# Performance work log

Hardware: AMD Instinct MI355X
Metric: run time of the kernel (lower is better)

The kernel has to match this reference:

```python
import jax, jax.numpy as jnp
import numpy as np

B, D, K, P = 4096, 510, 128, 332


def setup_inputs() -> dict:
    key = jax.random.key(0)
    k0, k1, k2, k3, k4 = jax.random.split(key, 5)
    z = jax.random.normal(k0, (B, D), dtype=jnp.float32)
    z_pre = jax.random.normal(k1, (B, D), dtype=jnp.float32)
    codebook = jax.random.normal(k2, (K, D), dtype=jnp.float32)
    phrase_table = jax.random.normal(k3, (P, D), dtype=jnp.float32)
    position_number = jax.random.randint(k4, (B,), 0, P, dtype=jnp.int64)
    return {"z": z, "z_pre": z_pre, "codebook": codebook,
            "phrase_table": phrase_table, "position_number": position_number}


def _vq(z, codebook):
    # squared L2 distance via ||z||^2 + ||c||^2 - 2 z.c  (same argmin as tf.norm)
    d2 = (jnp.sum(z * z, axis=-1, keepdims=True)
          + jnp.sum(codebook * codebook, axis=-1)[None, :]
          - 2.0 * jnp.einsum('bd,kd->bk', z, codebook))  # [B, K]
    k = jnp.argmin(d2, axis=-1)                           # [B]
    return codebook[k]                                    # gather -> [B, D]


def reference(z, z_pre, codebook, phrase_table, position_number):
    z_q = _vq(z, codebook)
    z_pre_q = _vq(z_pre, codebook)
    phrase_emb = phrase_table[position_number]            # [B, D]
    combined = z_q + z_pre_q + phrase_emb                 # decoder input in original model
    return combined
```

## Files before the change

### kernel.cpp

```cpp
#include <hip/hip_runtime.h>


#define BHALF 4096
#define D 510
#define K_CODES 128
#define CHB 32768
#define NCHUNK 8
#define GRID 512

using f32x4  = __attribute__((ext_vector_type(4))) float;
using bf16x8 = __attribute__((ext_vector_type(8))) short;

__device__ __forceinline__ unsigned short f2bf(float f) {
    union { float f; unsigned int u; } v; v.f = f;
    return (unsigned short)((v.u + 0x7FFFu + ((v.u >> 16) & 1u)) >> 16);
}
__device__ __forceinline__ float bf2f(unsigned short h) {
    union { unsigned int u; float f; } v; v.u = ((unsigned int)h) << 16;
    return v.f;
}
__device__ __forceinline__ bool lexlt(float va, int ia, float vb, int ib) {
    return va < vb || (va == vb && ia < ib);
}
#define MFMA16 __builtin_amdgcn_mfma_f32_16x16x32_bf16

__global__ void prep_kernel(const float* __restrict__ cb,
                            float* __restrict__ cnorm,
                            char* __restrict__ img) {
    const int code = blockIdx.x;
    const int l = threadIdx.x;
    const int swz = (code & 7) << 4;
    float s = 0.f;
    #pragma unroll
    for (int i = 0; i < 8; ++i) {
        const int k = l + 64 * i;
        const float v = (k < D) ? cb[(size_t)code * D + k] : 0.f;
        s = fmaf(v, v, s);
        const unsigned short hi = f2bf(v);
        const unsigned short lo = f2bf(v - bf2f(hi));
        char* base = img + (size_t)(k >> 6) * CHB + code * 256;
        const int off = (((k & 63) * 2) ^ swz);
        *(unsigned short*)(base + off) = hi;
        *(unsigned short*)(base + 128 + off) = lo;
    }
    #pragma unroll
    for (int m = 1; m < 64; m <<= 1) s += __shfl_xor(s, m, 64);
    if (l == 0) cnorm[code] = s;
}

__launch_bounds__(512, 4)
__global__ void main_kernel(const float* __restrict__ z,
                            const float* __restrict__ zp,
                            const float* __restrict__ cb,
                            const float* __restrict__ ph,
                            const int* __restrict__ pos,
                            const float* __restrict__ cnorm,
                            const char* __restrict__ img,
                            float* __restrict__ out) {
    __shared__ __align__(1024) char lds[65536];

    const int tid  = threadIdx.x;
    const int lane = tid & 63;
    const int wu   = __builtin_amdgcn_readfirstlane(tid >> 6);
    const int l15  = lane & 15;
    const int kq   = lane >> 4;
    const int r0   = blockIdx.x * 8;
    const int code = wu * 16 + l15;
    const int swz  = (l15 & 7) << 4;
    const float cn0 = cnorm[code];

    #pragma unroll
    for (int i = 0; i < 4; ++i) {
        const int u = tid + 512 * i;
        const int row = u >> 7;
        const int col = (u & 127) * 4;
        const float* src = (row < 8) ? z + (size_t)(r0 + row) * D
                                     : zp + (size_t)(r0 + row - 8) * D;
        const float2 va = *(const float2*)(src + col);
        const float2 vb = (col + 2 < D) ? *(const float2*)(src + col + 2)
                                        : make_float2(0.f, 0.f);
        const unsigned short h0 = f2bf(va.x), h1 = f2bf(va.y),
                             h2 = f2bf(vb.x), h3 = f2bf(vb.y);
        const unsigned short g0 = f2bf(va.x - bf2f(h0)), g1 = f2bf(va.y - bf2f(h1)),
                             g2 = f2bf(vb.x - bf2f(h2)), g3 = f2bf(vb.y - bf2f(h3));
        uint2 hi2, lo2;
        hi2.x = (unsigned)h0 | ((unsigned)h1 << 16);
        hi2.y = (unsigned)h2 | ((unsigned)h3 << 16);
        lo2.x = (unsigned)g0 | ((unsigned)g1 << 16);
        lo2.y = (unsigned)g2 | ((unsigned)g3 << 16);
        const int off = row * 1024 + ((col * 2) ^ ((row & 7) << 4));
        *(uint2*)(lds + off) = hi2;
        *(uint2*)(lds + 16384 + off) = lo2;
    }

    f32x4 acc = {0.f, 0.f, 0.f, 0.f};
    const char* zh0 = lds + l15 * 1024;
    const char* zl0 = lds + 16384 + l15 * 1024;
    const char* cbrow = lds + 32768 + code * 256;

    for (int c = 0; c < NCHUNK; ++c) {
        __syncthreads();
        {
            const char* g = img + (size_t)c * CHB;
            #pragma unroll
            for (int i = 0; i < 4; ++i) {
                const int u = i * 512 + tid;
                __builtin_amdgcn_global_load_lds(
                    (const __attribute__((address_space(1))) void*)(g + (size_t)u * 16),
                    (__attribute__((address_space(3))) void*)
                        (lds + 32768 + (size_t)(i * 512 + (tid & ~63)) * 16),
                    16, 0, 0);
            }
        }
        __syncthreads();
        #pragma unroll
        for (int ks = 0; ks < 2; ++ks) {
            const int kzB = (c * 128 + ks * 64 + kq * 16) ^ swz;
            const int kcB = (ks * 64 + kq * 16) ^ swz;
            const bf16x8 a_h = *(const bf16x8*)(zh0 + kzB);
            const bf16x8 a_l = *(const bf16x8*)(zl0 + kzB);
            const bf16x8 b_h = *(const bf16x8*)(cbrow + kcB);
            const bf16x8 b_l = *(const bf16x8*)(cbrow + 128 + kcB);
            acc = MFMA16(a_h, b_h, acc, 0, 0, 0);
            acc = MFMA16(a_h, b_l, acc, 0, 0, 0);
            acc = MFMA16(a_l, b_h, acc, 0, 0, 0);
        }
    }
    __syncthreads();

    float* tv1 = (float*)(lds);
    int*   ti1 = (int*)  (lds + 512);
    float* tv2 = (float*)(lds + 1024);
    int*   ti2 = (int*)  (lds + 1536);
    int*   i1a = (int*)  (lds + 2048);
    int*   i2a = (int*)  (lds + 2112);
    float* refd= (float*)(lds + 2176);
    int*   kbf = (int*)  (lds + 2304);

    #pragma unroll
    for (int j = 0; j < 4; ++j) {
        float v1 = cn0 - 2.f * acc[j];
        int   i1 = code;
        float v2 = 3.4e38f;
        int   i2 = 1 << 30;
        #pragma unroll
        for (int m = 1; m < 16; m <<= 1) {
            const float o1 = __shfl_xor(v1, m, 64); const int oi1 = __shfl_xor(i1, m, 64);
            const float o2 = __shfl_xor(v2, m, 64); const int oi2 = __shfl_xor(i2, m, 64);
            if (lexlt(o1, oi1, v1, i1)) {
                if (lexlt(v1, i1, o2, oi2)) { v2 = v1; i2 = i1; }
                else                        { v2 = o2; i2 = oi2; }
                v1 = o1; i1 = oi1;
            } else if (lexlt(o1, oi1, v2, i2)) { v2 = o1; i2 = oi1; }
        }
        if (l15 == 0) {
            const int mrow = kq * 4 + j;
            tv1[wu * 16 + mrow] = v1; ti1[wu * 16 + mrow] = i1;
            tv2[wu * 16 + mrow] = v2; ti2[wu * 16 + mrow] = i2;
        }
    }
    __syncthreads();

    if (tid < 16) {
        float v1 = tv1[tid]; int i1 = ti1[tid];
        float v2 = tv2[tid]; int i2 = ti2[tid];
        #pragma unroll
        for (int w = 1; w < 8; ++w) {
            const float o1 = tv1[w * 16 + tid], o2 = tv2[w * 16 + tid];
            const int  oi1 = ti1[w * 16 + tid], oi2 = ti2[w * 16 + tid];
            if (lexlt(o1, oi1, v1, i1)) {
                if (lexlt(v1, i1, o2, oi2)) { v2 = v1; i2 = i1; }
                else                        { v2 = o2; i2 = oi2; }
                v1 = o1; i1 = oi1;
            } else if (lexlt(o1, oi1, v2, i2)) { v2 = o1; i2 = oi1; }
        }
        i1a[tid] = i1; i2a[tid] = i2;
    }
    __syncthreads();

    {
        const int job = tid >> 4;
        const int l16 = tid & 15;
        const int row = job >> 1;
        const int cand = (job & 1) ? i2a[row] : i1a[row];
        const float* zr = (row < 8) ? z + (size_t)(r0 + row) * D
                                    : zp + (size_t)(r0 + row - 8) * D;
        const float* cr = cb + (size_t)cand * D;
        float dot = 0.f;
        #pragma unroll
        for (int t = 0; t < 16; ++t) {
            const int col = l16 * 2 + t * 32;
            if (col < D) {
                const float2 a = *(const float2*)(zr + col);
                const float2 b = *(const float2*)(cr + col);
                dot = fmaf(a.x, b.x, fmaf(a.y, b.y, dot));
            }
        }
        #pragma unroll
        for (int m = 1; m < 16; m <<= 1) dot += __shfl_xor(dot, m, 64);
        if (l16 == 0) refd[job] = cnorm[cand] - 2.f * dot;
    }
    __syncthreads();
    if (tid < 16) {
        const float da = refd[tid * 2], db = refd[tid * 2 + 1];
        const int ia = i1a[tid], ib = i2a[tid];
        kbf[tid] = lexlt(db, ib, da, ia) ? ib : ia;
    }
    __syncthreads();

    {
        const int grow = wu;
        const int kz   = kbf[grow];
        const int kzp2 = kbf[8 + grow];
        const int pp   = pos[r0 + grow];
        const float* ra = cb + (size_t)kz * D;
        const float* rb = cb + (size_t)kzp2 * D;
        const float* rp = ph + (size_t)pp * D;
        float* ro = out + (size_t)(r0 + grow) * D;
        #pragma unroll
        for (int q = 0; q < 4; ++q) {
            const int col = lane * 8 + q * 2;
            if (col < D) {
                const float2 a = *(const float2*)(ra + col);
                const float2 b = *(const float2*)(rb + col);
                const float2 p = *(const float2*)(rp + col);
                float2 o; o.x = a.x + b.x + p.x; o.y = a.y + b.y + p.y;
                *(float2*)(ro + col) = o;
            }
        }
    }
}

extern "C" void kernel_launch(void* const* d_in, const int* in_sizes, int n_in,
                              void* d_out, int out_size, void* d_ws, size_t ws_size,
                              hipStream_t stream) {
    const float* z  = (const float*)d_in[0];
    const float* zp = (const float*)d_in[1];
    const float* cb = (const float*)d_in[2];
    const float* ph = (const float*)d_in[3];
    const int*   pos = (const int*)d_in[4];
    float* out = (float*)d_out;

    float* cnorm = (float*)d_ws;
    char*  img   = (char*)d_ws + 512;

    prep_kernel<<<K_CODES, 64, 0, stream>>>(cb, cnorm, img);
    main_kernel<<<GRID, 512, 0, stream>>>(z, zp, cb, ph, pos, cnorm, img, out);
}
```

Before: 30.74 us.

## Fuse codebook preprocessing into main kernel with register-prefetched chunk conversion

Removes the separate prep kernel that built a bf16 hi/lo codebook image and codebook norms in workspace. Each block now loads fp32 codebook chunks into registers, prefetching the next chunk during the MFMA work on the current one, converts them to split bf16 in LDS, and computes the norms itself. This saves one kernel launch and the workspace round trip. In exchange, all 512 blocks redo the codebook conversion and there is an extra barrier per chunk.

```diff
diff --git a/kernel.cpp b/kernel.cpp
--- a/kernel.cpp
+++ b/kernel.cpp
@@ -3,9 +3,6 @@
 
 #define BHALF 4096
 #define D 510
-#define K_CODES 128
-#define CHB 32768
-#define NCHUNK 8
 #define GRID 512
 
 using f32x4  = __attribute__((ext_vector_type(4))) float;
@@ -24,40 +21,14 @@
 }
 #define MFMA16 __builtin_amdgcn_mfma_f32_16x16x32_bf16
 
-__global__ void prep_kernel(const float* __restrict__ cb,
-                            float* __restrict__ cnorm,
-                            char* __restrict__ img) {
-    const int code = blockIdx.x;
-    const int l = threadIdx.x;
-    const int swz = (code & 7) << 4;
-    float s = 0.f;
-    #pragma unroll
-    for (int i = 0; i < 8; ++i) {
-        const int k = l + 64 * i;
-        const float v = (k < D) ? cb[(size_t)code * D + k] : 0.f;
-        s = fmaf(v, v, s);
-        const unsigned short hi = f2bf(v);
-        const unsigned short lo = f2bf(v - bf2f(hi));
-        char* base = img + (size_t)(k >> 6) * CHB + code * 256;
-        const int off = (((k & 63) * 2) ^ swz);
-        *(unsigned short*)(base + off) = hi;
-        *(unsigned short*)(base + 128 + off) = lo;
-    }
-    #pragma unroll
-    for (int m = 1; m < 64; m <<= 1) s += __shfl_xor(s, m, 64);
-    if (l == 0) cnorm[code] = s;
-}
-
 __launch_bounds__(512, 4)
-__global__ void main_kernel(const float* __restrict__ z,
-                            const float* __restrict__ zp,
-                            const float* __restrict__ cb,
-                            const float* __restrict__ ph,
-                            const int* __restrict__ pos,
-                            const float* __restrict__ cnorm,
-                            const char* __restrict__ img,
-                            float* __restrict__ out) {
-    __shared__ __align__(1024) char lds[65536];
+__global__ void fused_kernel(const float* __restrict__ z,
+                             const float* __restrict__ zp,
+                             const float* __restrict__ cb,
+                             const float* __restrict__ ph,
+                             const int* __restrict__ pos,
+                             float* __restrict__ out) {
+    __shared__ __align__(1024) char lds[66048];
 
     const int tid  = threadIdx.x;
     const int lane = tid & 63;
@@ -66,8 +37,61 @@
     const int kq   = lane >> 4;
     const int r0   = blockIdx.x * 8;
     const int code = wu * 16 + l15;
-    const int swz  = (l15 & 7) << 4;
-    const float cn0 = cnorm[code];
+    const int swzB = (l15 & 7) << 4;
+
+    const int ct   = tid >> 2;
+    const int ks16 = (tid & 3) * 16;
+    const int cswz = (ct & 7) << 4;
+    const float* cg = cb + (size_t)ct * D;
+    char* cbase = lds + 32768 + ct * 256;
+    const int o0 = (ks16 * 2) ^ cswz;
+    const int o1 = ((ks16 * 2) + 16) ^ cswz;
+
+    float vr[16];
+    float sq = 0.f;
+
+#define CONVW() do {                                                          \
+        unsigned short h_[16], g_[16];                                        \
+        _Pragma("unroll")                                                     \
+        for (int j_ = 0; j_ < 16; ++j_) {                                     \
+            sq = fmaf(vr[j_], vr[j_], sq);                                    \
+            h_[j_] = f2bf(vr[j_]);                                            \
+            g_[j_] = f2bf(vr[j_] - bf2f(h_[j_]));                             \
+        }                                                                     \
+        uint4 H0 = make_uint4((unsigned)h_[0]|((unsigned)h_[1]<<16),          \
+                              (unsigned)h_[2]|((unsigned)h_[3]<<16),          \
+                              (unsigned)h_[4]|((unsigned)h_[5]<<16),          \
+                              (unsigned)h_[6]|((unsigned)h_[7]<<16));         \
+        uint4 H1 = make_uint4((unsigned)h_[8]|((unsigned)h_[9]<<16),          \
+                              (unsigned)h_[10]|((unsigned)h_[11]<<16),        \
+                              (unsigned)h_[12]|((unsigned)h_[13]<<16),        \
+                              (unsigned)h_[14]|((unsigned)h_[15]<<16));       \
+        uint4 L0 = make_uint4((unsigned)g_[0]|((unsigned)g_[1]<<16),          \
+                              (unsigned)g_[2]|((unsigned)g_[3]<<16),          \
+                              (unsigned)g_[4]|((unsigned)g_[5]<<16),          \
+                              (unsigned)g_[6]|((unsigned)g_[7]<<16));         \
+        uint4 L1 = make_uint4((unsigned)g_[8]|((unsigned)g_[9]<<16),          \
+                              (unsigned)g_[10]|((unsigned)g_[11]<<16),        \
+                              (unsigned)g_[12]|((unsigned)g_[13]<<16),        \
+                              (unsigned)g_[14]|((unsigned)g_[15]<<16));       \
+        *(uint4*)(cbase + o0) = H0;                                           \
+        *(uint4*)(cbase + o1) = H1;                                           \
+        *(uint4*)(cbase + 128 + o0) = L0;                                     \
+        *(uint4*)(cbase + 128 + o1) = L1;                                     \
+    } while (0)
+
+#define LOADC(cc) do {                                                        \
+        const int k0_ = (cc) * 64 + ks16;                                     \
+        _Pragma("unroll")                                                     \
+        for (int p_ = 0; p_ < 8; ++p_) {                                      \
+            const int col_ = k0_ + 2 * p_;                                    \
+            float2 t2_ = (col_ < D) ? *(const float2*)(cg + col_)             \
+                                    : make_float2(0.f, 0.f);                  \
+            vr[2*p_] = t2_.x; vr[2*p_+1] = t2_.y;                             \
+        }                                                                     \
+    } while (0)
+
+    LOADC(0);
 
     #pragma unroll
     for (int i = 0; i < 4; ++i) {
@@ -93,30 +117,20 @@
         *(uint2*)(lds + 16384 + off) = lo2;
     }
 
+    CONVW();
+    __syncthreads();
+
     f32x4 acc = {0.f, 0.f, 0.f, 0.f};
     const char* zh0 = lds + l15 * 1024;
     const char* zl0 = lds + 16384 + l15 * 1024;
     const char* cbrow = lds + 32768 + code * 256;
 
-    for (int c = 0; c < NCHUNK; ++c) {
-        __syncthreads();
-        {
-            const char* g = img + (size_t)c * CHB;
-            #pragma unroll
-            for (int i = 0; i < 4; ++i) {
-                const int u = i * 512 + tid;
-                __builtin_amdgcn_global_load_lds(
-                    (const __attribute__((address_space(1))) void*)(g + (size_t)u * 16),
-                    (__attribute__((address_space(3))) void*)
-                        (lds + 32768 + (size_t)(i * 512 + (tid & ~63)) * 16),
-                    16, 0, 0);
-            }
-        }
-        __syncthreads();
+    for (int c = 0; c < 8; ++c) {
+        if (c < 7) LOADC(c + 1);
         #pragma unroll
         for (int ks = 0; ks < 2; ++ks) {
-            const int kzB = (c * 128 + ks * 64 + kq * 16) ^ swz;
-            const int kcB = (ks * 64 + kq * 16) ^ swz;
+            const int kzB = (c * 128 + ks * 64 + kq * 16) ^ swzB;
+            const int kcB = (ks * 64 + kq * 16) ^ swzB;
             const bf16x8 a_h = *(const bf16x8*)(zh0 + kzB);
             const bf16x8 a_l = *(const bf16x8*)(zl0 + kzB);
             const bf16x8 b_h = *(const bf16x8*)(cbrow + kcB);
@@ -125,7 +139,15 @@
             acc = MFMA16(a_h, b_l, acc, 0, 0, 0);
             acc = MFMA16(a_l, b_h, acc, 0, 0, 0);
         }
-    }
+        __syncthreads();
+        if (c < 7) CONVW();
+        __syncthreads();
+    }
+
+    sq += __shfl_xor(sq, 1, 64);
+    sq += __shfl_xor(sq, 2, 64);
+    float* cn = (float*)(lds + 65536);
+    if ((tid & 3) == 0) cn[ct] = sq;
     __syncthreads();
 
     float* tv1 = (float*)(lds);
@@ -137,6 +159,7 @@
     float* refd= (float*)(lds + 2176);
     int*   kbf = (int*)  (lds + 2304);
 
+    const float cn0 = cn[code];
     #pragma unroll
     for (int j = 0; j < 4; ++j) {
         float v1 = cn0 - 2.f * acc[j];
@@ -145,13 +168,13 @@
         int   i2 = 1 << 30;
         #pragma unroll
         for (int m = 1; m < 16; m <<= 1) {
-            const float o1 = __shfl_xor(v1, m, 64); const int oi1 = __shfl_xor(i1, m, 64);
-            const float o2 = __shfl_xor(v2, m, 64); const int oi2 = __shfl_xor(i2, m, 64);
-            if (lexlt(o1, oi1, v1, i1)) {
-                if (lexlt(v1, i1, o2, oi2)) { v2 = v1; i2 = i1; }
-                else                        { v2 = o2; i2 = oi2; }
-                v1 = o1; i1 = oi1;
-            } else if (lexlt(o1, oi1, v2, i2)) { v2 = o1; i2 = oi1; }
+            const float o1v = __shfl_xor(v1, m, 64); const int oi1 = __shfl_xor(i1, m, 64);
+            const float o2v = __shfl_xor(v2, m, 64); const int oi2 = __shfl_xor(i2, m, 64);
+            if (lexlt(o1v, oi1, v1, i1)) {
+                if (lexlt(v1, i1, o2v, oi2)) { v2 = v1; i2 = i1; }
+                else                         { v2 = o2v; i2 = oi2; }
+                v1 = o1v; i1 = oi1;
+            } else if (lexlt(o1v, oi1, v2, i2)) { v2 = o1v; i2 = oi1; }
         }
         if (l15 == 0) {
             const int mrow = kq * 4 + j;
@@ -166,13 +189,13 @@
         float v2 = tv2[tid]; int i2 = ti2[tid];
         #pragma unroll
         for (int w = 1; w < 8; ++w) {
-            const float o1 = tv1[w * 16 + tid], o2 = tv2[w * 16 + tid];
+            const float o1v = tv1[w * 16 + tid], o2v = tv2[w * 16 + tid];
             const int  oi1 = ti1[w * 16 + tid], oi2 = ti2[w * 16 + tid];
-            if (lexlt(o1, oi1, v1, i1)) {
-                if (lexlt(v1, i1, o2, oi2)) { v2 = v1; i2 = i1; }
-                else                        { v2 = o2; i2 = oi2; }
-                v1 = o1; i1 = oi1;
-            } else if (lexlt(o1, oi1, v2, i2)) { v2 = o1; i2 = oi1; }
+            if (lexlt(o1v, oi1, v1, i1)) {
+                if (lexlt(v1, i1, o2v, oi2)) { v2 = v1; i2 = i1; }
+                else                         { v2 = o2v; i2 = oi2; }
+                v1 = o1v; i1 = oi1;
+            } else if (lexlt(o1v, oi1, v2, i2)) { v2 = o1v; i2 = oi1; }
         }
         i1a[tid] = i1; i2a[tid] = i2;
     }
@@ -198,7 +221,7 @@
         }
         #pragma unroll
         for (int m = 1; m < 16; m <<= 1) dot += __shfl_xor(dot, m, 64);
-        if (l16 == 0) refd[job] = cnorm[cand] - 2.f * dot;
+        if (l16 == 0) refd[job] = cn[cand] - 2.f * dot;
     }
     __syncthreads();
     if (tid < 16) {
@@ -229,6 +252,8 @@
             }
         }
     }
+#undef CONVW
+#undef LOADC
 }
 
 extern "C" void kernel_launch(void* const* d_in, const int* in_sizes, int n_in,
@@ -241,9 +266,5 @@
     const int*   pos = (const int*)d_in[4];
     float* out = (float*)d_out;
 
-    float* cnorm = (float*)d_ws;
-    char*  img   = (char*)d_ws + 512;
-
-    prep_kernel<<<K_CODES, 64, 0, stream>>>(cb, cnorm, img);
-    main_kernel<<<GRID, 512, 0, stream>>>(z, zp, cb, ph, pos, cnorm, img, out);
-}
+    fused_kernel<<<GRID, 512, 0, stream>>>(z, zp, cb, ph, pos, out);
+}
```

New measurement: 30.57 us. No clear change (-0.6%).

## Fuse codebook prep into main kernel and use single-bf16 MFMA with top-4 fp32 rescoring

Applied to the files above, without the earlier changes.

Removes the separate prep kernel. Each block now converts the whole codebook to bf16 in LDS and computes code norms itself. The hi/lo split-bf16 triple MFMA is replaced by a single bf16 MFMA pass, with accuracy recovered by keeping the top-4 candidates per row and rescoring them exactly in fp32. This saves one launch and two thirds of the MFMA work, but each block redundantly reconverts the full codebook and uses about 150KB of LDS, which limits occupancy to one block per CU.

```diff
diff --git a/kernel.cpp b/kernel.cpp
--- a/kernel.cpp
+++ b/kernel.cpp
@@ -3,9 +3,6 @@
 
 #define BHALF 4096
 #define D 510
-#define K_CODES 128
-#define CHB 32768
-#define NCHUNK 8
 #define GRID 512
 
 using f32x4  = __attribute__((ext_vector_type(4))) float;
@@ -15,49 +12,29 @@
     union { float f; unsigned int u; } v; v.f = f;
     return (unsigned short)((v.u + 0x7FFFu + ((v.u >> 16) & 1u)) >> 16);
 }
-__device__ __forceinline__ float bf2f(unsigned short h) {
-    union { unsigned int u; float f; } v; v.u = ((unsigned int)h) << 16;
-    return v.f;
-}
 __device__ __forceinline__ bool lexlt(float va, int ia, float vb, int ib) {
     return va < vb || (va == vb && ia < ib);
 }
 #define MFMA16 __builtin_amdgcn_mfma_f32_16x16x32_bf16
 
-__global__ void prep_kernel(const float* __restrict__ cb,
-                            float* __restrict__ cnorm,
-                            char* __restrict__ img) {
-    const int code = blockIdx.x;
-    const int l = threadIdx.x;
-    const int swz = (code & 7) << 4;
-    float s = 0.f;
-    #pragma unroll
-    for (int i = 0; i < 8; ++i) {
-        const int k = l + 64 * i;
-        const float v = (k < D) ? cb[(size_t)code * D + k] : 0.f;
-        s = fmaf(v, v, s);
-        const unsigned short hi = f2bf(v);
-        const unsigned short lo = f2bf(v - bf2f(hi));
-        char* base = img + (size_t)(k >> 6) * CHB + code * 256;
-        const int off = (((k & 63) * 2) ^ swz);
-        *(unsigned short*)(base + off) = hi;
-        *(unsigned short*)(base + 128 + off) = lo;
-    }
-    #pragma unroll
-    for (int m = 1; m < 64; m <<= 1) s += __shfl_xor(s, m, 64);
-    if (l == 0) cnorm[code] = s;
-}
-
-__launch_bounds__(512, 4)
-__global__ void main_kernel(const float* __restrict__ z,
-                            const float* __restrict__ zp,
-                            const float* __restrict__ cb,
-                            const float* __restrict__ ph,
-                            const int* __restrict__ pos,
-                            const float* __restrict__ cnorm,
-                            const char* __restrict__ img,
-                            float* __restrict__ out) {
-    __shared__ __align__(1024) char lds[65536];
+#define LCB   0
+#define LZ    131072
+#define LCN   147456
+#define LTWV  147968
+#define LTWI  150016
+#define LKB2  152064
+#define LREFD 152320
+#define LKBF  152576
+#define LDSZ  152640
+
+__launch_bounds__(512)
+__global__ void fused_kernel(const float* __restrict__ z,
+                             const float* __restrict__ zp,
+                             const float* __restrict__ cb,
+                             const float* __restrict__ ph,
+                             const int* __restrict__ pos,
+                             float* __restrict__ out) {
+    __shared__ __align__(1024) char lds[LDSZ];
 
     const int tid  = threadIdx.x;
     const int lane = tid & 63;
@@ -65,146 +42,176 @@
     const int l15  = lane & 15;
     const int kq   = lane >> 4;
     const int r0   = blockIdx.x * 8;
-    const int code = wu * 16 + l15;
-    const int swz  = (l15 & 7) << 4;
-    const float cn0 = cnorm[code];
-
-    #pragma unroll
-    for (int i = 0; i < 4; ++i) {
-        const int u = tid + 512 * i;
-        const int row = u >> 7;
-        const int col = (u & 127) * 4;
+
+    float* cnL = (float*)(lds + LCN);
+
+    {
+        const int ct    = tid >> 2;
+        const int kbase = (tid & 3) * 128;
+        const int cswz  = (ct & 7) << 4;
+        const float* cg = cb + (size_t)ct * D;
+        char* cbase = lds + LCB + ct * 1024;
+        float sq = 0.f;
+        #pragma unroll
+        for (int g = 0; g < 8; ++g) {
+            const int k0 = kbase + g * 16;
+            float v[16];
+            #pragma unroll
+            for (int p = 0; p < 8; ++p) {
+                const int col = k0 + 2 * p;
+                const float2 t2 = (col < D) ? *(const float2*)(cg + col)
+                                            : make_float2(0.f, 0.f);
+                v[2 * p] = t2.x; v[2 * p + 1] = t2.y;
+            }
+            unsigned short h[16];
+            #pragma unroll
+            for (int j = 0; j < 16; ++j) {
+                sq = fmaf(v[j], v[j], sq);
+                h[j] = f2bf(v[j]);
+            }
+            uint4 H0 = make_uint4((unsigned)h[0]|((unsigned)h[1]<<16),
+                                  (unsigned)h[2]|((unsigned)h[3]<<16),
+                                  (unsigned)h[4]|((unsigned)h[5]<<16),
+                                  (unsigned)h[6]|((unsigned)h[7]<<16));
+            uint4 H1 = make_uint4((unsigned)h[8]|((unsigned)h[9]<<16),
+                                  (unsigned)h[10]|((unsigned)h[11]<<16),
+                                  (unsigned)h[12]|((unsigned)h[13]<<16),
+                                  (unsigned)h[14]|((unsigned)h[15]<<16));
+            *(uint4*)(cbase + ((k0 * 2) ^ cswz))      = H0;
+            *(uint4*)(cbase + ((k0 * 2 + 16) ^ cswz)) = H1;
+        }
+        sq += __shfl_xor(sq, 1, 64);
+        sq += __shfl_xor(sq, 2, 64);
+        if ((tid & 3) == 0) cnL[ct] = sq;
+    }
+
+    {
+        const int row  = tid >> 5;
+        const int k0   = (tid & 31) * 16;
+        const int rswz = (row & 7) << 4;
         const float* src = (row < 8) ? z + (size_t)(r0 + row) * D
                                      : zp + (size_t)(r0 + row - 8) * D;
-        const float2 va = *(const float2*)(src + col);
-        const float2 vb = (col + 2 < D) ? *(const float2*)(src + col + 2)
+        float v[16];
+        #pragma unroll
+        for (int p = 0; p < 8; ++p) {
+            const int col = k0 + 2 * p;
+            const float2 t2 = (col < D) ? *(const float2*)(src + col)
                                         : make_float2(0.f, 0.f);
-        const unsigned short h0 = f2bf(va.x), h1 = f2bf(va.y),
-                             h2 = f2bf(vb.x), h3 = f2bf(vb.y);
-        const unsigned short g0 = f2bf(va.x - bf2f(h0)), g1 = f2bf(va.y - bf2f(h1)),
-                             g2 = f2bf(vb.x - bf2f(h2)), g3 = f2bf(vb.y - bf2f(h3));
-        uint2 hi2, lo2;
-        hi2.x = (unsigned)h0 | ((unsigned)h1 << 16);
-        hi2.y = (unsigned)h2 | ((unsigned)h3 << 16);
-        lo2.x = (unsigned)g0 | ((unsigned)g1 << 16);
-        lo2.y = (unsigned)g2 | ((unsigned)g3 << 16);
-        const int off = row * 1024 + ((col * 2) ^ ((row & 7) << 4));
-        *(uint2*)(lds + off) = hi2;
-        *(uint2*)(lds + 16384 + off) = lo2;
-    }
+            v[2 * p] = t2.x; v[2 * p + 1] = t2.y;
+        }
+        unsigned short h[16];
+        #pragma unroll
+        for (int j = 0; j < 16; ++j) h[j] = f2bf(v[j]);
+        uint4 H0 = make_uint4((unsigned)h[0]|((unsigned)h[1]<<16),
+                              (unsigned)h[2]|((unsigned)h[3]<<16),
+                              (unsigned)h[4]|((unsigned)h[5]<<16),
+                              (unsigned)h[6]|((unsigned)h[7]<<16));
+        uint4 H1 = make_uint4((unsigned)h[8]|((unsigned)h[9]<<16),
+                              (unsigned)h[10]|((unsigned)h[11]<<16),
+                              (unsigned)h[12]|((unsigned)h[13]<<16),
+                              (unsigned)h[14]|((unsigned)h[15]<<16));
+        char* zbase = lds + LZ + row * 1024;
+        *(uint4*)(zbase + ((k0 * 2) ^ rswz))      = H0;
+        *(uint4*)(zbase + ((k0 * 2 + 16) ^ rswz)) = H1;
+    }
+    __syncthreads();
 
     f32x4 acc = {0.f, 0.f, 0.f, 0.f};
-    const char* zh0 = lds + l15 * 1024;
-    const char* zl0 = lds + 16384 + l15 * 1024;
-    const char* cbrow = lds + 32768 + code * 256;
-
-    for (int c = 0; c < NCHUNK; ++c) {
-        __syncthreads();
-        {
-            const char* g = img + (size_t)c * CHB;
-            #pragma unroll
-            for (int i = 0; i < 4; ++i) {
-                const int u = i * 512 + tid;
-                __builtin_amdgcn_global_load_lds(
-                    (const __attribute__((address_space(1))) void*)(g + (size_t)u * 16),
-                    (__attribute__((address_space(3))) void*)
-                        (lds + 32768 + (size_t)(i * 512 + (tid & ~63)) * 16),
-                    16, 0, 0);
-            }
-        }
-        __syncthreads();
-        #pragma unroll
-        for (int ks = 0; ks < 2; ++ks) {
-            const int kzB = (c * 128 + ks * 64 + kq * 16) ^ swz;
-            const int kcB = (ks * 64 + kq * 16) ^ swz;
-            const bf16x8 a_h = *(const bf16x8*)(zh0 + kzB);
-            const bf16x8 a_l = *(const bf16x8*)(zl0 + kzB);
-            const bf16x8 b_h = *(const bf16x8*)(cbrow + kcB);
-            const bf16x8 b_l = *(const bf16x8*)(cbrow + 128 + kcB);
-            acc = MFMA16(a_h, b_h, acc, 0, 0, 0);
-            acc = MFMA16(a_h, b_l, acc, 0, 0, 0);
-            acc = MFMA16(a_l, b_h, acc, 0, 0, 0);
-        }
-    }
-    __syncthreads();
-
-    float* tv1 = (float*)(lds);
-    int*   ti1 = (int*)  (lds + 512);
-    float* tv2 = (float*)(lds + 1024);
-    int*   ti2 = (int*)  (lds + 1536);
-    int*   i1a = (int*)  (lds + 2048);
-    int*   i2a = (int*)  (lds + 2112);
-    float* refd= (float*)(lds + 2176);
-    int*   kbf = (int*)  (lds + 2304);
-
+    const int code = wu * 16 + l15;
+    const int swzB = (l15 & 7) << 4;
+    const char* za = lds + LZ + l15 * 1024;
+    const char* ba = lds + LCB + code * 1024;
+    #pragma unroll
+    for (int s = 0; s < 16; ++s) {
+        const int kb = (s * 64 + kq * 16) ^ swzB;
+        const bf16x8 a = *(const bf16x8*)(za + kb);
+        const bf16x8 b = *(const bf16x8*)(ba + kb);
+        acc = MFMA16(a, b, acc, 0, 0, 0);
+    }
+
+    float* twv = (float*)(lds + LTWV);
+    int*   twi = (int*)(lds + LTWI);
+    const float cnv = cnL[code];
     #pragma unroll
     for (int j = 0; j < 4; ++j) {
-        float v1 = cn0 - 2.f * acc[j];
-        int   i1 = code;
-        float v2 = 3.4e38f;
-        int   i2 = 1 << 30;
-        #pragma unroll
-        for (int m = 1; m < 16; m <<= 1) {
-            const float o1 = __shfl_xor(v1, m, 64); const int oi1 = __shfl_xor(i1, m, 64);
-            const float o2 = __shfl_xor(v2, m, 64); const int oi2 = __shfl_xor(i2, m, 64);
-            if (lexlt(o1, oi1, v1, i1)) {
-                if (lexlt(v1, i1, o2, oi2)) { v2 = v1; i2 = i1; }
-                else                        { v2 = o2; i2 = oi2; }
-                v1 = o1; i1 = oi1;
-            } else if (lexlt(o1, oi1, v2, i2)) { v2 = o1; i2 = oi1; }
-        }
-        if (l15 == 0) {
-            const int mrow = kq * 4 + j;
-            tv1[wu * 16 + mrow] = v1; ti1[wu * 16 + mrow] = i1;
-            tv2[wu * 16 + mrow] = v2; ti2[wu * 16 + mrow] = i2;
-        }
-    }
-    __syncthreads();
-
-    if (tid < 16) {
-        float v1 = tv1[tid]; int i1 = ti1[tid];
-        float v2 = tv2[tid]; int i2 = ti2[tid];
-        #pragma unroll
-        for (int w = 1; w < 8; ++w) {
-            const float o1 = tv1[w * 16 + tid], o2 = tv2[w * 16 + tid];
-            const int  oi1 = ti1[w * 16 + tid], oi2 = ti2[w * 16 + tid];
-            if (lexlt(o1, oi1, v1, i1)) {
-                if (lexlt(v1, i1, o2, oi2)) { v2 = v1; i2 = i1; }
-                else                        { v2 = o2; i2 = oi2; }
-                v1 = o1; i1 = oi1;
-            } else if (lexlt(o1, oi1, v2, i2)) { v2 = o1; i2 = oi1; }
-        }
-        i1a[tid] = i1; i2a[tid] = i2;
-    }
-    __syncthreads();
-
-    {
-        const int job = tid >> 4;
-        const int l16 = tid & 15;
-        const int row = job >> 1;
-        const int cand = (job & 1) ? i2a[row] : i1a[row];
+        float vv = cnv - 2.f * acc[j];
+        int   vi = code;
+        const int row = kq * 4 + j;
+        #pragma unroll
+        for (int t = 0; t < 4; ++t) {
+            float mv = vv; int mi = vi;
+            #pragma unroll
+            for (int m = 1; m < 16; m <<= 1) {
+                const float ov = __shfl_xor(mv, m, 64);
+                const int   oi = __shfl_xor(mi, m, 64);
+                if (lexlt(ov, oi, mv, mi)) { mv = ov; mi = oi; }
+            }
+            if (l15 == 0) {
+                twv[(wu * 16 + row) * 4 + t] = mv;
+                twi[(wu * 16 + row) * 4 + t] = mi;
+            }
+            if (vi == mi) { vv = 3.4e38f; vi = 0x7fffffff; }
+        }
+    }
+    __syncthreads();
+
+    int* kb2 = (int*)(lds + LKB2);
+    {
+        const int row = tid >> 5;
+        const int c32 = tid & 31;
+        float vv = twv[((c32 >> 2) * 16 + row) * 4 + (c32 & 3)];
+        int   vi = twi[((c32 >> 2) * 16 + row) * 4 + (c32 & 3)];
+        #pragma unroll
+        for (int t = 0; t < 4; ++t) {
+            float mv = vv; int mi = vi;
+            #pragma unroll
+            for (int m = 1; m < 32; m <<= 1) {
+                const float ov = __shfl_xor(mv, m, 64);
+                const int   oi = __shfl_xor(mi, m, 64);
+                if (lexlt(ov, oi, mv, mi)) { mv = ov; mi = oi; }
+            }
+            if (c32 == 0) kb2[row * 4 + t] = mi;
+            if (vi == mi) { vv = 3.4e38f; vi = 0x7fffffff; }
+        }
+    }
+    __syncthreads();
+
+    float* refd = (float*)(lds + LREFD);
+    {
+        const int job = tid >> 3;
+        const int l8  = tid & 7;
+        const int row = job >> 2;
+        const int cand = kb2[row * 4 + (job & 3)];
         const float* zr = (row < 8) ? z + (size_t)(r0 + row) * D
                                     : zp + (size_t)(r0 + row - 8) * D;
         const float* cr = cb + (size_t)cand * D;
         float dot = 0.f;
         #pragma unroll
-        for (int t = 0; t < 16; ++t) {
-            const int col = l16 * 2 + t * 32;
+        for (int it = 0; it < 32; ++it) {
+            const int col = l8 * 2 + it * 16;
             if (col < D) {
                 const float2 a = *(const float2*)(zr + col);
                 const float2 b = *(const float2*)(cr + col);
                 dot = fmaf(a.x, b.x, fmaf(a.y, b.y, dot));
             }
         }
-        #pragma unroll
-        for (int m = 1; m < 16; m <<= 1) dot += __shfl_xor(dot, m, 64);
-        if (l16 == 0) refd[job] = cnorm[cand] - 2.f * dot;
-    }
-    __syncthreads();
+        dot += __shfl_xor(dot, 1, 64);
+        dot += __shfl_xor(dot, 2, 64);
+        dot += __shfl_xor(dot, 4, 64);
+        if (l8 == 0) refd[job] = cnL[cand] - 2.f * dot;
+    }
+    __syncthreads();
+
+    int* kbf = (int*)(lds + LKBF);
     if (tid < 16) {
-        const float da = refd[tid * 2], db = refd[tid * 2 + 1];
-        const int ia = i1a[tid], ib = i2a[tid];
-        kbf[tid] = lexlt(db, ib, da, ia) ? ib : ia;
+        float bd = refd[tid * 4]; int bi = kb2[tid * 4];
+        #pragma unroll
+        for (int q = 1; q < 4; ++q) {
+            const float d = refd[tid * 4 + q];
+            const int   i = kb2[tid * 4 + q];
+            if (lexlt(d, i, bd, bi)) { bd = d; bi = i; }
+        }
+        kbf[tid] = bi;
     }
     __syncthreads();
 
@@ -241,9 +248,5 @@
     const int*   pos = (const int*)d_in[4];
     float* out = (float*)d_out;
 
-    float* cnorm = (float*)d_ws;
-    char*  img   = (char*)d_ws + 512;
-
-    prep_kernel<<<K_CODES, 64, 0, stream>>>(cb, cnorm, img);
-    main_kernel<<<GRID, 512, 0, stream>>>(z, zp, cb, ph, pos, cnorm, img, out);
-}
+    fused_kernel<<<GRID, 512, 0, stream>>>(z, zp, cb, ph, pos, out);
+}
```

After: 51.12 us. +66.3%, slower.
